# Performance work log

Hardware: AMD Instinct MI355X
Metric: run time of the kernel (lower is better)

The kernel has to match this reference:

```python
import jax, jax.numpy as jnp
import numpy as np

N_FFT = 1024
HOP_LENGTH = 480
NB_MAX_FRAMES = 1000
N_MELS = 64
SPEC_WIDTH = 1024
N_BINS = N_FFT // 2 + 1  # 513


def setup_inputs() -> dict:
    key = jax.random.key(0)
    B, L = 32, 480000  # 10 s @ 48 kHz -> 1001 frames, truncated to 1000
    waveform = jax.random.normal(key, (B, L), dtype=jnp.float32)

    # DFT-as-conv weights, exactly as in the torch module (hann periodic window)
    n = np.arange(N_FFT, dtype=np.float32)
    window = 0.5 - 0.5 * np.cos(2.0 * np.pi * n / N_FFT)  # torch.hann_window (periodic)
    k = np.arange(N_BINS, dtype=np.float32)[:, None]
    angle = 2.0 * np.pi * k * n[None, :] / N_FFT
    stft_weights = np.concatenate(
        [window * np.cos(angle), -window * np.sin(angle)], axis=0
    ).astype(np.float32)  # [2*N_BINS, N_FFT]

    # Stand-in for HF's slaney mel filterbank (513 -> 64): non-negative, sparse-ish scale
    mel_filters = jax.random.uniform(
        jax.random.fold_in(key, 1), (N_BINS, N_MELS), dtype=jnp.float32
    ) * 0.02

    return {
        "waveform": waveform,
        "stft_weights": jnp.asarray(stft_weights),
        "mel_filters": mel_filters,
    }


def _bilinear_align_corners(img, out_h, out_w):
    """F.interpolate(mode='bilinear', align_corners=True) on [B,C,H,W]."""
    B, C, H, W = img.shape

    def coords(out, inn):
        scale = (inn - 1) / max(out - 1, 1)
        pos = jnp.arange(out, dtype=jnp.float32) * scale
        i0 = jnp.clip(jnp.floor(pos).astype(jnp.int32), 0, inn - 1)
        return i0, pos - i0.astype(jnp.float32)

    h0, hw = coords(out_h, H)
    w0, ww = coords(out_w, W)
    h1 = jnp.minimum(h0 + 1, H - 1)
    w1 = jnp.minimum(w0 + 1, W - 1)

    rows = (img[:, :, h0, :] * (1.0 - hw)[None, None, :, None]
            + img[:, :, h1, :] * hw[None, None, :, None])  # [B,C,out_h,W]
    out = rows[..., w0] * (1.0 - ww) + rows[..., w1] * ww   # [B,C,out_h,out_w]
    return out


def reference(waveform, stft_weights, mel_filters):
    pad = N_FFT // 2
    x = jnp.pad(waveform, ((0, 0), (pad, pad)), mode="reflect")  # center=True

    # strided conv1d == frame extraction + GEMM with the DFT matrix
    T = (x.shape[1] - N_FFT) // HOP_LENGTH + 1
    idx = jnp.arange(T)[:, None] * HOP_LENGTH + jnp.arange(N_FFT)[None, :]
    frames = x[:, idx]                                   # [B, T, N_FFT]
    spec = jnp.einsum("btn,kn->bkt", frames, stft_weights)  # [B, 2*N_BINS, T]

    real = spec[:, :N_BINS, :]
    imag = spec[:, N_BINS:, :]
    power = (real * real + imag * imag)[:, :, :NB_MAX_FRAMES]  # [B, 513, 1000]

    mel = jnp.einsum("bft,fm->bmt", power, mel_filters)        # [B, 64, 1000]
    log_mel = 10.0 * jnp.log10(jnp.clip(mel, 1e-10))

    img = jnp.transpose(log_mel, (0, 2, 1))[:, None]           # [B, 1, 1000, 64]
    return _bilinear_align_corners(img, SPEC_WIDTH, N_MELS)    # [B, 1, 1024, 64]
```

## Files before the change

### kernel.cpp

```cpp
#include <hip/hip_runtime.h>
#include <hip/hip_bf16.h>

#define LWAV   480000
#define XPADL  481024
#define NBATCH 32
#define TOUT   1000
#define MTOT   32000
#define NFFT   1024
#define NBINS  513
#define NMEL   64
#define PSTR   576
#define SPECW  1024
#define HOP    480

#define XPAD_OFF 0u
#define WB_OFF   30785536u
#define WMT_OFF  32886784u
#define PW_OFF   32960512u
#define LM_OFF   69824512u

typedef __attribute__((ext_vector_type(8))) __bf16 bf16x8;
typedef __attribute__((ext_vector_type(4))) float  f32x4;

__device__ __forceinline__ void gload16(const void* g, void* l) {
  __builtin_amdgcn_global_load_lds((const __attribute__((address_space(1))) void*)g,
                                   (__attribute__((address_space(3))) void*)l, 16, 0, 0);
}

#define NV1 (NBATCH * (XPADL / 8))
#define NV2 ((1026 * NFFT) / 8)
#define NV3 (NMEL * (PSTR / 8))

__global__ void prep_kernel(const float* __restrict__ wav,
                            const float* __restrict__ wstft,
                            const float* __restrict__ mf,
                            unsigned char* __restrict__ ws) {
  __hip_bfloat16* xpad = (__hip_bfloat16*)(ws + XPAD_OFF);
  __hip_bfloat16* wb   = (__hip_bfloat16*)(ws + WB_OFF);
  __hip_bfloat16* wmt  = (__hip_bfloat16*)(ws + WMT_OFF);
  int idx = blockIdx.x * blockDim.x + threadIdx.x;
  if (idx < NV1) {
    int b  = idx / (XPADL / 8);
    int pg = (idx - b * (XPADL / 8)) * 8;
    __hip_bfloat16* dst = xpad + (size_t)b * XPADL + pg;
    const float* src = wav + (size_t)b * LWAV;
    if (pg >= 512 && pg <= LWAV + 496) {
      float4 v0 = *(const float4*)(src + pg - 512);
      float4 v1 = *(const float4*)(src + pg - 508);
      __hip_bfloat16 t[8];
      t[0] = __float2bfloat16(v0.x); t[1] = __float2bfloat16(v0.y);
      t[2] = __float2bfloat16(v0.z); t[3] = __float2bfloat16(v0.w);
      t[4] = __float2bfloat16(v1.x); t[5] = __float2bfloat16(v1.y);
      t[6] = __float2bfloat16(v1.z); t[7] = __float2bfloat16(v1.w);
      *(uint4*)dst = *(const uint4*)t;
    } else {
      for (int j = 0; j < 8; ++j) {
        int s = pg + j - 512;
        if (s < 0) s = -s;
        else if (s >= LWAV) s = 2 * (LWAV - 1) - s;
        dst[j] = __float2bfloat16(src[s]);
      }
    }
  } else if (idx < NV1 + NV2) {
    int g = (idx - NV1) * 8;
    float4 v0 = *(const float4*)(wstft + g);
    float4 v1 = *(const float4*)(wstft + g + 4);
    __hip_bfloat16 t[8];
    t[0] = __float2bfloat16(v0.x); t[1] = __float2bfloat16(v0.y);
    t[2] = __float2bfloat16(v0.z); t[3] = __float2bfloat16(v0.w);
    t[4] = __float2bfloat16(v1.x); t[5] = __float2bfloat16(v1.y);
    t[6] = __float2bfloat16(v1.z); t[7] = __float2bfloat16(v1.w);
    *(uint4*)(wb + g) = *(const uint4*)t;
  } else if (idx < NV1 + NV2 + NV3) {
    int j  = idx - NV1 - NV2;
    int n  = j / (PSTR / 8);
    int k0 = (j - n * (PSTR / 8)) * 8;
    for (int k = k0; k < k0 + 8; ++k)
      wmt[n * PSTR + k] = __float2bfloat16(k < NBINS ? mf[k * NMEL + n] : 0.0f);
  }
}

#define STFT_NWG (9 * 250)
__launch_bounds__(256, 2)
__global__ void stft_kernel(unsigned char* __restrict__ ws) {
  __shared__ __align__(16) unsigned char sA[128 * 128];
  __shared__ __align__(16) unsigned char sB[128 * 128];
  const unsigned char* xpadb = ws + XPAD_OFF;
  const unsigned char* wbb   = ws + WB_OFF;
  __hip_bfloat16* pw = (__hip_bfloat16*)(ws + PW_OFF);

  const int tid = threadIdx.x;
  const int lane = tid & 63;
  const int wid  = tid >> 6;

  const int orig = blockIdx.x;
  const int q = STFT_NWG / 8, r = STFT_NWG % 8;
  const int xcd = orig & 7;
  const int w = (xcd < r ? xcd * (q + 1) : r * (q + 1) + (xcd - r) * q) + (orig >> 3);
  const int f0 = (w % 9) * 64;
  const int m0 = (w / 9) * 128;

  const int wm = (wid >> 1) * 64;
  const int wf = (wid & 1) * 32;

  const int srow = lane >> 3;
  const int kb2  = (lane & 7) << 4;

  const unsigned char* aptr[4];
  const unsigned char* bptr[4];
  unsigned char* aldst[4];
  unsigned char* bldst[4];
#pragma unroll
  for (int j = 0; j < 4; ++j) {
    int rr = wid * 32 + j * 8 + srow;
    int m = m0 + rr;
    int bb = m / 1000;
    int t  = m - bb * 1000;
    aptr[j] = xpadb + ((size_t)bb * XPADL + (size_t)t * HOP) * 2 + (kb2 ^ ((rr & 7) << 4));
    aldst[j] = &sA[(wid * 32 + j * 8) * 128];
    int wr = (rr < 64) ? (f0 + rr) : (513 + f0 + (rr - 64));
    if (wr > 1025) wr = 1025;
    bptr[j] = wbb + (size_t)wr * (NFFT * 2) + (kb2 ^ ((rr & 7) << 4));
    bldst[j] = &sB[(wid * 32 + j * 8) * 128];
  }

  f32x4 accC[4][2], accS[4][2];
#pragma unroll
  for (int mi = 0; mi < 4; ++mi)
#pragma unroll
    for (int fr = 0; fr < 2; ++fr) {
      accC[mi][fr] = (f32x4){0.f, 0.f, 0.f, 0.f};
      accS[mi][fr] = (f32x4){0.f, 0.f, 0.f, 0.f};
    }

  for (int kk = 0; kk < NFFT; kk += 64) {
    __syncthreads();
#pragma unroll
    for (int j = 0; j < 4; ++j) gload16(aptr[j] + (size_t)kk * 2, aldst[j]);
#pragma unroll
    for (int j = 0; j < 4; ++j) gload16(bptr[j] + (size_t)kk * 2, bldst[j]);
    __syncthreads();
#pragma unroll
    for (int ks = 0; ks < 2; ++ks) {
      const int kby = ks * 64 + ((lane >> 4) << 4);
      bf16x8 af[4], bc[2], bs[2];
#pragma unroll
      for (int mi = 0; mi < 4; ++mi) {
        int rr = wm + mi * 16 + (lane & 15);
        af[mi] = *(const bf16x8*)&sA[rr * 128 + (kby ^ ((rr & 7) << 4))];
      }
#pragma unroll
      for (int fr = 0; fr < 2; ++fr) {
        int rc = wf + fr * 16 + (lane & 15);
        int sw = kby ^ ((rc & 7) << 4);
        bc[fr] = *(const bf16x8*)&sB[rc * 128 + sw];
        bs[fr] = *(const bf16x8*)&sB[(64 + rc) * 128 + sw];
      }
#pragma unroll
      for (int mi = 0; mi < 4; ++mi)
#pragma unroll
        for (int fr = 0; fr < 2; ++fr) {
          accC[mi][fr] = __builtin_amdgcn_mfma_f32_16x16x32_bf16(af[mi], bc[fr], accC[mi][fr], 0, 0, 0);
          accS[mi][fr] = __builtin_amdgcn_mfma_f32_16x16x32_bf16(af[mi], bs[fr], accS[mi][fr], 0, 0, 0);
        }
    }
  }

  const int col = lane & 15;
  const int rg  = lane >> 4;
#pragma unroll
  for (int mi = 0; mi < 4; ++mi)
#pragma unroll
    for (int fr = 0; fr < 2; ++fr) {
      int f = f0 + wf + fr * 16 + col;
#pragma unroll
      for (int rr = 0; rr < 4; ++rr) {
        int m = m0 + wm + mi * 16 + rg * 4 + rr;
        float c = accC[mi][fr][rr];
        float s = accS[mi][fr][rr];
        float p = (f < NBINS) ? (c * c + s * s) : 0.0f;
        pw[(size_t)m * PSTR + f] = __float2bfloat16(p);
      }
    }
}

__launch_bounds__(256, 2)
__global__ void mel_kernel(unsigned char* __restrict__ ws) {
  __shared__ __align__(16) unsigned char sA[128 * 128];
  __shared__ __align__(16) unsigned char sBt[64 * 128];
  const unsigned char* pwb  = ws + PW_OFF;
  const unsigned char* wmtb = ws + WMT_OFF;
  float* lm = (float*)(ws + LM_OFF);

  const int tid = threadIdx.x;
  const int lane = tid & 63;
  const int wid  = tid >> 6;
  const int m0 = blockIdx.x * 128;

  const int srow = lane >> 3;
  const int kb2  = (lane & 7) << 4;

  const unsigned char* aptr[4];
  unsigned char* aldst[4];
#pragma unroll
  for (int j = 0; j < 4; ++j) {
    int rr = wid * 32 + j * 8 + srow;
    aptr[j] = pwb + (size_t)(m0 + rr) * (PSTR * 2) + (kb2 ^ ((rr & 7) << 4));
    aldst[j] = &sA[(wid * 32 + j * 8) * 128];
  }
  const unsigned char* bptr[2];
  unsigned char* bldst[2];
#pragma unroll
  for (int j = 0; j < 2; ++j) {
    int rr = wid * 16 + j * 8 + srow;
    bptr[j] = wmtb + (size_t)rr * (PSTR * 2) + (kb2 ^ ((rr & 7) << 4));
    bldst[j] = &sBt[(wid * 16 + j * 8) * 128];
  }

  f32x4 acc[2][4];
#pragma unroll
  for (int mi = 0; mi < 2; ++mi)
#pragma unroll
    for (int fr = 0; fr < 4; ++fr) acc[mi][fr] = (f32x4){0.f, 0.f, 0.f, 0.f};

  for (int kk = 0; kk < PSTR; kk += 64) {
    __syncthreads();
#pragma unroll
    for (int j = 0; j < 4; ++j) gload16(aptr[j] + (size_t)kk * 2, aldst[j]);
#pragma unroll
    for (int j = 0; j < 2; ++j) gload16(bptr[j] + (size_t)kk * 2, bldst[j]);
    __syncthreads();
#pragma unroll
    for (int ks = 0; ks < 2; ++ks) {
      const int kby = ks * 64 + ((lane >> 4) << 4);
      bf16x8 af[2], bfr[4];
#pragma unroll
      for (int mi = 0; mi < 2; ++mi) {
        int rr = wid * 32 + mi * 16 + (lane & 15);
        af[mi] = *(const bf16x8*)&sA[rr * 128 + (kby ^ ((rr & 7) << 4))];
      }
#pragma unroll
      for (int fr = 0; fr < 4; ++fr) {
        int rr = fr * 16 + (lane & 15);
        bfr[fr] = *(const bf16x8*)&sBt[rr * 128 + (kby ^ ((rr & 7) << 4))];
      }
#pragma unroll
      for (int mi = 0; mi < 2; ++mi)
#pragma unroll
        for (int fr = 0; fr < 4; ++fr)
          acc[mi][fr] = __builtin_amdgcn_mfma_f32_16x16x32_bf16(af[mi], bfr[fr], acc[mi][fr], 0, 0, 0);
    }
  }

  const int col = lane & 15;
  const int rg  = lane >> 4;
#pragma unroll
  for (int mi = 0; mi < 2; ++mi)
#pragma unroll
    for (int fr = 0; fr < 4; ++fr) {
      int n = fr * 16 + col;
#pragma unroll
      for (int rr = 0; rr < 4; ++rr) {
        int m = m0 + wid * 32 + mi * 16 + rg * 4 + rr;
        float v = acc[mi][fr][rr];
        lm[(size_t)m * NMEL + n] = 10.0f * log10f(fmaxf(v, 1e-10f));
      }
    }
}

__global__ void interp_kernel(const unsigned char* __restrict__ ws, float* __restrict__ out) {
  const float* lm = (const float*)(ws + LM_OFF);
  int idx = blockIdx.x * blockDim.x + threadIdx.x;
  if (idx >= NBATCH * SPECW * 16) return;
  int m4 = idx & 15;
  int h  = (idx >> 4) & (SPECW - 1);
  int b  = idx >> 14;
  const float scale = (float)(999.0 / 1023.0);
  float pos = (float)h * scale;
  int i0 = (int)floorf(pos);
  if (i0 > TOUT - 1) i0 = TOUT - 1;
  float w = pos - (float)i0;
  int i1 = i0 + 1;
  if (i1 > TOUT - 1) i1 = TOUT - 1;
  const float4* r0 = (const float4*)(lm + ((size_t)b * TOUT + i0) * NMEL);
  const float4* r1 = (const float4*)(lm + ((size_t)b * TOUT + i1) * NMEL);
  float4 a = r0[m4], c = r1[m4];
  float4 o;
  o.x = a.x * (1.0f - w) + c.x * w;
  o.y = a.y * (1.0f - w) + c.y * w;
  o.z = a.z * (1.0f - w) + c.z * w;
  o.w = a.w * (1.0f - w) + c.w * w;
  ((float4*)out)[idx] = o;
}

extern "C" void kernel_launch(void* const* d_in, const int* in_sizes, int n_in,
                              void* d_out, int out_size, void* d_ws, size_t ws_size,
                              hipStream_t stream) {
  (void)in_sizes; (void)n_in; (void)out_size; (void)ws_size;
  const float* wav   = (const float*)d_in[0];
  const float* wstft = (const float*)d_in[1];
  const float* mf    = (const float*)d_in[2];
  unsigned char* ws  = (unsigned char*)d_ws;
  float* out = (float*)d_out;

  const int tot = NV1 + NV2 + NV3;
  prep_kernel<<<(tot + 255) / 256, 256, 0, stream>>>(wav, wstft, mf, ws);
  stft_kernel<<<STFT_NWG, 256, 0, stream>>>(ws);
  mel_kernel<<<250, 256, 0, stream>>>(ws);
  interp_kernel<<<(NBATCH * SPECW * 16) / 256, 256, 0, stream>>>(ws, out);
}
```

Baseline: 110.8 us.

## Restructure STFT GEMM into 256x256 double-buffered tiles and split off Nyquist bin

Rewrites the STFT GEMM to use 512-thread workgroups with 256-frame by 128-bin tiles. A 128KB LDS double buffer is filled with staggered async loads, explicit vmcnt waits and setprio around the MFMA bursts. The 513th (Nyquist) bin is removed from the main GEMM so the power matrix becomes exactly 512 wide with no padding. That bin is computed as a scalar dot product inside the mel kernel and added to the mel accumulation. The aim is to remove the wasted padding columns (576 vs 513) and raise data reuse and load/compute overlap, at the cost of higher register/LDS pressure and an extra serial dot loop in the mel kernel.

```diff
diff --git a/kernel.cpp b/kernel.cpp
--- a/kernel.cpp
+++ b/kernel.cpp
@@ -5,21 +5,21 @@
 #define XPADL  481024
 #define NBATCH 32
 #define TOUT   1000
-#define MTOT   32000
 #define NFFT   1024
 #define NBINS  513
 #define NMEL   64
-#define PSTR   576
+#define PWC    512
 #define SPECW  1024
 #define HOP    480
 
 #define XPAD_OFF 0u
 #define WB_OFF   30785536u
 #define WMT_OFF  32886784u
-#define PW_OFF   32960512u
-#define LM_OFF   69824512u
+#define PW_OFF   32952320u
+#define LM_OFF   65720320u
 
 typedef __attribute__((ext_vector_type(8))) __bf16 bf16x8;
+typedef __attribute__((ext_vector_type(8))) unsigned short ushort8;
 typedef __attribute__((ext_vector_type(4))) float  f32x4;
 
 __device__ __forceinline__ void gload16(const void* g, void* l) {
@@ -27,9 +27,12 @@
                                    (__attribute__((address_space(3))) void*)l, 16, 0, 0);
 }
 
+#define WAIT_VM(n) asm volatile("s_waitcnt vmcnt(" #n ")" ::: "memory")
+#define BAR() __builtin_amdgcn_s_barrier()
+
 #define NV1 (NBATCH * (XPADL / 8))
 #define NV2 ((1026 * NFFT) / 8)
-#define NV3 (NMEL * (PSTR / 8))
+#define NV3 ((NMEL * PWC) / 8)
 
 __global__ void prep_kernel(const float* __restrict__ wav,
                             const float* __restrict__ wstft,
@@ -73,123 +76,160 @@
     *(uint4*)(wb + g) = *(const uint4*)t;
   } else if (idx < NV1 + NV2 + NV3) {
     int j  = idx - NV1 - NV2;
-    int n  = j / (PSTR / 8);
-    int k0 = (j - n * (PSTR / 8)) * 8;
+    int n  = j / (PWC / 8);
+    int k0 = (j - n * (PWC / 8)) * 8;
     for (int k = k0; k < k0 + 8; ++k)
-      wmt[n * PSTR + k] = __float2bfloat16(k < NBINS ? mf[k * NMEL + n] : 0.0f);
-  }
-}
-
-#define STFT_NWG (9 * 250)
-__launch_bounds__(256, 2)
+      wmt[n * PWC + k] = __float2bfloat16(mf[k * NMEL + n]);
+  }
+}
+
+#define STFT_NWG 500
+__launch_bounds__(512, 2)
 __global__ void stft_kernel(unsigned char* __restrict__ ws) {
-  __shared__ __align__(16) unsigned char sA[128 * 128];
-  __shared__ __align__(16) unsigned char sB[128 * 128];
+  __shared__ __align__(16) unsigned char lds[131072];
   const unsigned char* xpadb = ws + XPAD_OFF;
   const unsigned char* wbb   = ws + WB_OFF;
   __hip_bfloat16* pw = (__hip_bfloat16*)(ws + PW_OFF);
 
-  const int tid = threadIdx.x;
+  const int tid  = threadIdx.x;
   const int lane = tid & 63;
-  const int wid  = tid >> 6;
+  const int w    = tid >> 6;
+  const int wm   = w >> 2;
+  const int wc   = w & 3;
 
   const int orig = blockIdx.x;
-  const int q = STFT_NWG / 8, r = STFT_NWG % 8;
+  const int q8 = STFT_NWG / 8, r8 = STFT_NWG % 8;
   const int xcd = orig & 7;
-  const int w = (xcd < r ? xcd * (q + 1) : r * (q + 1) + (xcd - r) * q) + (orig >> 3);
-  const int f0 = (w % 9) * 64;
-  const int m0 = (w / 9) * 128;
-
-  const int wm = (wid >> 1) * 64;
-  const int wf = (wid & 1) * 32;
-
-  const int srow = lane >> 3;
-  const int kb2  = (lane & 7) << 4;
-
-  const unsigned char* aptr[4];
-  const unsigned char* bptr[4];
-  unsigned char* aldst[4];
-  unsigned char* bldst[4];
-#pragma unroll
-  for (int j = 0; j < 4; ++j) {
-    int rr = wid * 32 + j * 8 + srow;
-    int m = m0 + rr;
-    int bb = m / 1000;
-    int t  = m - bb * 1000;
-    aptr[j] = xpadb + ((size_t)bb * XPADL + (size_t)t * HOP) * 2 + (kb2 ^ ((rr & 7) << 4));
-    aldst[j] = &sA[(wid * 32 + j * 8) * 128];
-    int wr = (rr < 64) ? (f0 + rr) : (513 + f0 + (rr - 64));
-    if (wr > 1025) wr = 1025;
-    bptr[j] = wbb + (size_t)wr * (NFFT * 2) + (kb2 ^ ((rr & 7) << 4));
-    bldst[j] = &sB[(wid * 32 + j * 8) * 128];
-  }
-
-  f32x4 accC[4][2], accS[4][2];
-#pragma unroll
-  for (int mi = 0; mi < 4; ++mi)
-#pragma unroll
-    for (int fr = 0; fr < 2; ++fr) {
-      accC[mi][fr] = (f32x4){0.f, 0.f, 0.f, 0.f};
-      accS[mi][fr] = (f32x4){0.f, 0.f, 0.f, 0.f};
-    }
-
-  for (int kk = 0; kk < NFFT; kk += 64) {
-    __syncthreads();
-#pragma unroll
-    for (int j = 0; j < 4; ++j) gload16(aptr[j] + (size_t)kk * 2, aldst[j]);
-#pragma unroll
-    for (int j = 0; j < 4; ++j) gload16(bptr[j] + (size_t)kk * 2, bldst[j]);
-    __syncthreads();
-#pragma unroll
-    for (int ks = 0; ks < 2; ++ks) {
-      const int kby = ks * 64 + ((lane >> 4) << 4);
-      bf16x8 af[4], bc[2], bs[2];
-#pragma unroll
-      for (int mi = 0; mi < 4; ++mi) {
-        int rr = wm + mi * 16 + (lane & 15);
-        af[mi] = *(const bf16x8*)&sA[rr * 128 + (kby ^ ((rr & 7) << 4))];
-      }
-#pragma unroll
-      for (int fr = 0; fr < 2; ++fr) {
-        int rc = wf + fr * 16 + (lane & 15);
-        int sw = kby ^ ((rc & 7) << 4);
-        bc[fr] = *(const bf16x8*)&sB[rc * 128 + sw];
-        bs[fr] = *(const bf16x8*)&sB[(64 + rc) * 128 + sw];
-      }
-#pragma unroll
-      for (int mi = 0; mi < 4; ++mi)
-#pragma unroll
-        for (int fr = 0; fr < 2; ++fr) {
-          accC[mi][fr] = __builtin_amdgcn_mfma_f32_16x16x32_bf16(af[mi], bc[fr], accC[mi][fr], 0, 0, 0);
-          accS[mi][fr] = __builtin_amdgcn_mfma_f32_16x16x32_bf16(af[mi], bs[fr], accS[mi][fr], 0, 0, 0);
+  const int wg = (xcd < r8 ? xcd * (q8 + 1) : r8 * (q8 + 1) + (xcd - r8) * q8) + (orig >> 3);
+  const int bin0 = (wg & 3) * 128;
+  const int m0   = (wg >> 2) * 256;
+
+  const int srow = tid >> 3;
+  const int scol = (tid & 7) << 4;
+
+  const unsigned char *gA0, *gA1, *gA2, *gA3, *gB0, *gB1, *gB2, *gB3;
+  {
+    int r0 = srow, r1 = 64 + srow, r2 = 128 + srow, r3 = 192 + srow;
+    int m, bb, tt;
+    m = m0 + r0; bb = m / 1000; tt = m - bb * 1000;
+    gA0 = xpadb + ((size_t)bb * XPADL + (size_t)tt * HOP) * 2 + (scol ^ ((r0 & 7) << 4));
+    m = m0 + r1; bb = m / 1000; tt = m - bb * 1000;
+    gA1 = xpadb + ((size_t)bb * XPADL + (size_t)tt * HOP) * 2 + (scol ^ ((r1 & 7) << 4));
+    m = m0 + r2; bb = m / 1000; tt = m - bb * 1000;
+    gA2 = xpadb + ((size_t)bb * XPADL + (size_t)tt * HOP) * 2 + (scol ^ ((r2 & 7) << 4));
+    m = m0 + r3; bb = m / 1000; tt = m - bb * 1000;
+    gA3 = xpadb + ((size_t)bb * XPADL + (size_t)tt * HOP) * 2 + (scol ^ ((r3 & 7) << 4));
+#define BROW(r) ((size_t)(bin0 + (((r) >> 5) << 4) + ((r) & 15) + ((((r) >> 4) & 1) * 513)) * 2048)
+    gB0 = wbb + BROW(r0) + (scol ^ ((r0 & 7) << 4));
+    gB1 = wbb + BROW(r1) + (scol ^ ((r1 & 7) << 4));
+    gB2 = wbb + BROW(r2) + (scol ^ ((r2 & 7) << 4));
+    gB3 = wbb + BROW(r3) + (scol ^ ((r3 & 7) << 4));
+  }
+
+#define LDSA(c, qq) ((void*)(lds + (c) * 32768 + (qq) * 8192 + w * 1024))
+#define LDSB(c, qq) ((void*)(lds + 65536 + (c) * 32768 + (qq) * 8192 + w * 1024))
+#define STG_B01(c, kb) do { gload16(gB0 + (kb), LDSB(c, 0)); gload16(gB1 + (kb), LDSB(c, 1)); } while (0)
+#define STG_B23(c, kb) do { gload16(gB2 + (kb), LDSB(c, 2)); gload16(gB3 + (kb), LDSB(c, 3)); } while (0)
+#define STG_A02(c, kb) do { gload16(gA0 + (kb), LDSA(c, 0)); gload16(gA2 + (kb), LDSA(c, 2)); } while (0)
+#define STG_A13(c, kb) do { gload16(gA1 + (kb), LDSA(c, 1)); gload16(gA3 + (kb), LDSA(c, 3)); } while (0)
+
+  f32x4 acc[8][4];
+#pragma unroll
+  for (int a = 0; a < 8; ++a)
+#pragma unroll
+    for (int b = 0; b < 4; ++b) acc[a][b] = (f32x4){0.f, 0.f, 0.f, 0.f};
+
+  STG_B01(0, 0); STG_B23(0, 0); STG_A02(0, 0); STG_A13(0, 0);
+  STG_B01(1, 128); STG_B23(1, 128); STG_A02(1, 128);
+  WAIT_VM(6);
+  BAR();
+
+  bf16x8 bfr[4][2];
+  bf16x8 af[2][2];
+
+  for (int i = 0; i < 8; ++i) {
+    const int kbO  = i * 256 + 128;
+    const int kbN  = i * 256 + 256;
+    const int kbN1 = i * 256 + 384;
+#pragma unroll
+    for (int ph = 0; ph < 8; ++ph) {
+      const int cc = ph >> 2;
+      const int qq = ph & 3;
+      const unsigned char* bA = lds + cc * 32768;
+      const unsigned char* bB = lds + 65536 + cc * 32768;
+      if (qq == 0) {
+#pragma unroll
+        for (int nf = 0; nf < 4; ++nf)
+#pragma unroll
+          for (int ks = 0; ks < 2; ++ks) {
+            int row = wc * 64 + nf * 16 + (lane & 15);
+            bfr[nf][ks] = *(const bf16x8*)(bB + row * 128 +
+                            ((ks * 64 + ((lane >> 4) << 4)) ^ ((row & 7) << 4)));
+          }
+      }
+#pragma unroll
+      for (int mi = 0; mi < 2; ++mi)
+#pragma unroll
+        for (int ks = 0; ks < 2; ++ks) {
+          int row = wm * 128 + (qq * 2 + mi) * 16 + (lane & 15);
+          af[mi][ks] = *(const bf16x8*)(bA + row * 128 +
+                          ((ks * 64 + ((lane >> 4) << 4)) ^ ((row & 7) << 4)));
         }
+      if (ph == 0) { STG_A13(1, kbO); }
+      if (i < 7) {
+        if (ph == 1) STG_B01(0, kbN);
+        if (ph == 2) STG_B23(0, kbN);
+        if (ph == 3) STG_A02(0, kbN);
+        if (ph == 4) STG_A13(0, kbN);
+        if (ph == 5) STG_B01(1, kbN1);
+        if (ph == 6) STG_B23(1, kbN1);
+        if (ph == 7) STG_A02(1, kbN1);
+      }
+      if (ph == 3) { if (i < 7) { WAIT_VM(6); } else { WAIT_VM(0); } }
+      if (ph == 7 && i < 7) { WAIT_VM(6); }
+      BAR();
+      __builtin_amdgcn_s_setprio(1);
+#pragma unroll
+      for (int mi = 0; mi < 2; ++mi)
+#pragma unroll
+        for (int nf = 0; nf < 4; ++nf) {
+          acc[qq * 2 + mi][nf] = __builtin_amdgcn_mfma_f32_16x16x32_bf16(
+              af[mi][0], bfr[nf][0], acc[qq * 2 + mi][nf], 0, 0, 0);
+          acc[qq * 2 + mi][nf] = __builtin_amdgcn_mfma_f32_16x16x32_bf16(
+              af[mi][1], bfr[nf][1], acc[qq * 2 + mi][nf], 0, 0, 0);
+        }
+      __builtin_amdgcn_s_setprio(0);
+      BAR();
     }
   }
 
   const int col = lane & 15;
   const int rg  = lane >> 4;
 #pragma unroll
-  for (int mi = 0; mi < 4; ++mi)
-#pragma unroll
-    for (int fr = 0; fr < 2; ++fr) {
-      int f = f0 + wf + fr * 16 + col;
+  for (int mf_ = 0; mf_ < 8; ++mf_)
+#pragma unroll
+    for (int g = 0; g < 2; ++g) {
+      int bin = bin0 + wc * 32 + g * 16 + col;
 #pragma unroll
       for (int rr = 0; rr < 4; ++rr) {
-        int m = m0 + wm + mi * 16 + rg * 4 + rr;
-        float c = accC[mi][fr][rr];
-        float s = accS[mi][fr][rr];
-        float p = (f < NBINS) ? (c * c + s * s) : 0.0f;
-        pw[(size_t)m * PSTR + f] = __float2bfloat16(p);
+        int m = m0 + wm * 128 + mf_ * 16 + rg * 4 + rr;
+        float c = acc[mf_][2 * g][rr];
+        float s = acc[mf_][2 * g + 1][rr];
+        pw[(size_t)m * PWC + bin] = __float2bfloat16(c * c + s * s);
       }
     }
 }
 
 __launch_bounds__(256, 2)
-__global__ void mel_kernel(unsigned char* __restrict__ ws) {
+__global__ void mel_kernel(unsigned char* __restrict__ ws, const float* __restrict__ mfp) {
   __shared__ __align__(16) unsigned char sA[128 * 128];
   __shared__ __align__(16) unsigned char sBt[64 * 128];
-  const unsigned char* pwb  = ws + PW_OFF;
-  const unsigned char* wmtb = ws + WMT_OFF;
+  __shared__ __align__(16) __hip_bfloat16 wrow[2][1024];
+  __shared__ float p512s[128];
+  const unsigned char* xpadb = ws + XPAD_OFF;
+  const unsigned char* wbb   = ws + WB_OFF;
+  const unsigned char* pwb   = ws + PW_OFF;
+  const unsigned char* wmtb  = ws + WMT_OFF;
   float* lm = (float*)(ws + LM_OFF);
 
   const int tid = threadIdx.x;
@@ -197,6 +237,29 @@
   const int wid  = tid >> 6;
   const int m0 = blockIdx.x * 128;
 
+  {
+    int rsel = tid >> 7;
+    int seg  = (tid & 127) * 16;
+    *(uint4*)((unsigned char*)wrow + rsel * 2048 + seg) =
+        *(const uint4*)(wbb + (size_t)(rsel ? 1025 : 512) * 2048 + seg);
+  }
+  __syncthreads();
+  {
+    int mloc = tid >> 1, part = tid & 1;
+    int m = m0 + mloc, bb = m / 1000, tt = m - bb * 1000;
+    const unsigned char* fb = xpadb + ((size_t)bb * XPADL + (size_t)tt * HOP) * 2;
+    float dot = 0.f;
+    for (int j = 0; j < 128; ++j) {
+      ushort8 fv = *(const ushort8*)(fb + j * 16);
+      ushort8 wv = *(const ushort8*)((const unsigned char*)wrow + part * 2048 + j * 16);
+#pragma unroll
+      for (int e = 0; e < 8; ++e)
+        dot += __uint_as_float((unsigned)fv[e] << 16) * __uint_as_float((unsigned)wv[e] << 16);
+    }
+    float od = __shfl_xor(dot, 1);
+    if (part == 0) p512s[mloc] = dot * dot + od * od;
+  }
+
   const int srow = lane >> 3;
   const int kb2  = (lane & 7) << 4;
 
@@ -205,7 +268,7 @@
 #pragma unroll
   for (int j = 0; j < 4; ++j) {
     int rr = wid * 32 + j * 8 + srow;
-    aptr[j] = pwb + (size_t)(m0 + rr) * (PSTR * 2) + (kb2 ^ ((rr & 7) << 4));
+    aptr[j] = pwb + (size_t)(m0 + rr) * (PWC * 2) + (kb2 ^ ((rr & 7) << 4));
     aldst[j] = &sA[(wid * 32 + j * 8) * 128];
   }
   const unsigned char* bptr[2];
@@ -213,7 +276,7 @@
 #pragma unroll
   for (int j = 0; j < 2; ++j) {
     int rr = wid * 16 + j * 8 + srow;
-    bptr[j] = wmtb + (size_t)rr * (PSTR * 2) + (kb2 ^ ((rr & 7) << 4));
+    bptr[j] = wmtb + (size_t)rr * (PWC * 2) + (kb2 ^ ((rr & 7) << 4));
     bldst[j] = &sBt[(wid * 16 + j * 8) * 128];
   }
 
@@ -223,7 +286,7 @@
 #pragma unroll
     for (int fr = 0; fr < 4; ++fr) acc[mi][fr] = (f32x4){0.f, 0.f, 0.f, 0.f};
 
-  for (int kk = 0; kk < PSTR; kk += 64) {
+  for (int kk = 0; kk < PWC; kk += 64) {
     __syncthreads();
 #pragma unroll
     for (int j = 0; j < 4; ++j) gload16(aptr[j] + (size_t)kk * 2, aldst[j]);
@@ -259,11 +322,12 @@
 #pragma unroll
     for (int fr = 0; fr < 4; ++fr) {
       int n = fr * 16 + col;
+      float f512 = mfp[512 * NMEL + n];
 #pragma unroll
       for (int rr = 0; rr < 4; ++rr) {
-        int m = m0 + wid * 32 + mi * 16 + rg * 4 + rr;
-        float v = acc[mi][fr][rr];
-        lm[(size_t)m * NMEL + n] = 10.0f * log10f(fmaxf(v, 1e-10f));
+        int mrow = wid * 32 + mi * 16 + rg * 4 + rr;
+        float v = acc[mi][fr][rr] + p512s[mrow] * f512;
+        lm[(size_t)(m0 + mrow) * NMEL + n] = 10.0f * log10f(fmaxf(v, 1e-10f));
       }
     }
 }
@@ -305,7 +369,7 @@
 
   const int tot = NV1 + NV2 + NV3;
   prep_kernel<<<(tot + 255) / 256, 256, 0, stream>>>(wav, wstft, mf, ws);
-  stft_kernel<<<STFT_NWG, 256, 0, stream>>>(ws);
-  mel_kernel<<<250, 256, 0, stream>>>(ws);
+  stft_kernel<<<STFT_NWG, 512, 0, stream>>>(ws);
+  mel_kernel<<<250, 256, 0, stream>>>(ws, mf);
   interp_kernel<<<(NBATCH * SPECW * 16) / 256, 256, 0, stream>>>(ws, out);
 }
```

Result: slower. 114.1 us (+3.0%).
